# Optimization experiments

Hardware: AMD Instinct MI355X
Metric: run time of the kernel (lower is better)

Reference implementation:

```python
import jax, jax.numpy as jnp
import numpy as np

B, L, D, DI, DS, DC, DTR = 128, 31, 1024, 2048, 16, 5, 64

def setup_inputs() -> dict:
    key = jax.random.key(0)
    ks = jax.random.split(key, 12)
    rn = lambda k, shp, s=0.02: jax.random.normal(k, shp, dtype=jnp.float32) * s
    return {
        "x": jax.random.normal(ks[0], (B, L, D), dtype=jnp.float32),
        "norm1_w": jnp.ones((D,), jnp.float32), "norm1_b": jnp.zeros((D,), jnp.float32),
        "in_proj_W": rn(ks[1], (2 * DI, D)),
        "conv_w": rn(ks[2], (DI, DC), 0.2), "conv_b": jnp.zeros((DI,), jnp.float32),
        "x_proj_W": rn(ks[3], (DTR + 2 * DS, DI)),
        "dt_proj_W": rn(ks[4], (DI, DTR), 0.1),
        "dt_proj_b": jnp.full((DI,), -4.6, dtype=jnp.float32),  # softplus^-1(~0.01)
        "A_log": jnp.tile(jnp.log(jnp.arange(1, DS + 1, dtype=jnp.float32))[None, :], (DI, 1)),
        "D_ssm": jnp.ones((DI,), jnp.float32),
        "out_proj_W": rn(ks[5], (D, DI)),
        "norm2_w": jnp.ones((D,), jnp.float32), "norm2_b": jnp.zeros((D,), jnp.float32),
        "ffn_W1": rn(ks[6], (2 * D, D)), "ffn_b1": jnp.zeros((2 * D,), jnp.float32),
        "ffn_W2": rn(ks[7], (D, 2 * D)), "ffn_b2": jnp.zeros((D,), jnp.float32),
        "cls_W1": rn(ks[8], (D, L * D)), "cls_b1": jnp.zeros((D,), jnp.float32),
        "cls_W2": rn(ks[9], (1, D)), "cls_b2": jnp.zeros((1,), jnp.float32),
    }

def _ln(x, w, b):
    m = x.mean(-1, keepdims=True)
    v = x.var(-1, keepdims=True)
    return (x - m) * jax.lax.rsqrt(v + 1e-5) * w + b

def _mamba(x, in_proj_W, conv_w, conv_b, x_proj_W, dt_proj_W, dt_proj_b, A_log, D_ssm, out_proj_W):
    # in_proj -> (u, z)
    xz = jnp.einsum('bld,ed->ble', x, in_proj_W)            # (B,L,2*DI)
    u, z = jnp.split(xz, 2, axis=-1)
    # causal depthwise conv1d (kernel DC) + SiLU
    xp = jnp.pad(u, ((0, 0), (DC - 1, 0), (0, 0)))
    uc = conv_b + sum(xp[:, k:k + L, :] * conv_w[:, k] for k in range(DC))
    uc = jax.nn.silu(uc)
    # input-dependent dt, B, C
    x_dbl = jnp.einsum('bld,ed->ble', uc, x_proj_W)         # (B,L,DTR+2*DS)
    dt, Bm, Cm = jnp.split(x_dbl, [DTR, DTR + DS], axis=-1)
    dt = jax.nn.softplus(jnp.einsum('blr,dr->bld', dt, dt_proj_W) + dt_proj_b)
    A = -jnp.exp(A_log)                                      # (DI,DS)
    def step(h, ins):
        dt_t, B_t, C_t, u_t = ins                            # (B,DI),(B,DS),(B,DS),(B,DI)
        dA = jnp.exp(dt_t[:, :, None] * A)                   # (B,DI,DS)
        h = h * dA + dt_t[:, :, None] * B_t[:, None, :] * u_t[:, :, None]
        y = jnp.einsum('bds,bs->bd', h, C_t)
        return h, y
    h0 = jnp.zeros((u.shape[0], DI, DS), u.dtype)
    _, ys = jax.lax.scan(step, h0, (dt.transpose(1, 0, 2), Bm.transpose(1, 0, 2),
                                    Cm.transpose(1, 0, 2), uc.transpose(1, 0, 2)))
    y = ys.transpose(1, 0, 2) + uc * D_ssm                   # skip term D*u
    y = y * jax.nn.silu(z)                                   # gate
    return jnp.einsum('bld,ed->ble', y, out_proj_W)

def reference(x, norm1_w, norm1_b, in_proj_W, conv_w, conv_b, x_proj_W, dt_proj_W,
              dt_proj_b, A_log, D_ssm, out_proj_W, norm2_w, norm2_b, ffn_W1, ffn_b1,
              ffn_W2, ffn_b2, cls_W1, cls_b1, cls_W2, cls_b2):
    # single encoder block (n_layers=1), dropout = identity (eval)
    res = x
    h = _ln(x, norm1_w, norm1_b)
    h = _mamba(h, in_proj_W, conv_w, conv_b, x_proj_W, dt_proj_W, dt_proj_b,
               A_log, D_ssm, out_proj_W)
    x = res + h
    res = x
    h = _ln(x, norm2_w, norm2_b)
    h = jax.nn.silu(jnp.einsum('bld,ed->ble', h, ffn_W1) + ffn_b1)
    h = jnp.einsum('ble,de->bld', h, ffn_W2) + ffn_b2
    x = res + h
    # classifier: Flatten -> Linear -> SiLU -> Linear
    flat = x.reshape(x.shape[0], -1)                          # (B, L*D)
    c = jax.nn.silu(flat @ cls_W1.T + cls_b1)
    out = c @ cls_W2.T + cls_b2                               # (B,1)
    return (out, x)
```

## Files before the change

kernel.cpp:

```cpp
#include <hip/hip_runtime.h>
#include <cstddef>
#include <cstdint>

#define B_   128
#define L_   31
#define D_   1024
#define DI_  2048
#define DS_  16
#define DC_  5
#define DTR_ 64
#define ROWS (B_ * L_)
#define KCLS (L_ * D_)

typedef unsigned short u16;
typedef __attribute__((ext_vector_type(8))) short s16x8;
typedef __attribute__((ext_vector_type(4))) float f32x4;

__device__ __forceinline__ float silu_f(float x) { return x / (1.0f + __expf(-x)); }

__device__ __forceinline__ u16 f2b(float f) {
    union { float f; uint32_t u; } c; c.f = f;
    uint32_t u = c.u + 0x7FFF + ((c.u >> 16) & 1);
    return (u16)(u >> 16);
}
__device__ __forceinline__ float b2f(u16 b) {
    union { uint32_t u; float f; } c; c.u = ((uint32_t)b) << 16;
    return c.f;
}
__device__ __forceinline__ uint32_t pack2(float lo, float hi) {
    return (uint32_t)f2b(lo) | ((uint32_t)f2b(hi) << 16);
}

#define GLD16(g, s) __builtin_amdgcn_global_load_lds( \
    (const __attribute__((address_space(1))) void*)(g), \
    (__attribute__((address_space(3))) void*)(s), 16, 0, 0)

__global__ __launch_bounds__(256) void f2b_kernel(const float* __restrict__ in,
                                                  u16* __restrict__ out, int n8)
{
    int i = blockIdx.x * 256 + threadIdx.x;
    if (i >= n8) return;
    const float4* p = (const float4*)in + (size_t)i * 2;
    float4 a = p[0], b = p[1];
    uint4 r;
    r.x = pack2(a.x, a.y); r.y = pack2(a.z, a.w);
    r.z = pack2(b.x, b.y); r.w = pack2(b.z, b.w);
    ((uint4*)out)[i] = r;
}

__global__ __launch_bounds__(256) void ln_kernel(const float* __restrict__ x,
                                                 const float* __restrict__ w,
                                                 const float* __restrict__ b,
                                                 u16* __restrict__ y)
{
    const int row = blockIdx.x;
    const float* xr = x + (size_t)row * D_;
    float v[4];
    float sum = 0.f, sq = 0.f;
#pragma unroll
    for (int i = 0; i < 4; i++) {
        v[i] = xr[threadIdx.x + i * 256];
        sum += v[i];
        sq  += v[i] * v[i];
    }
#pragma unroll
    for (int o = 32; o > 0; o >>= 1) {
        sum += __shfl_down(sum, o, 64);
        sq  += __shfl_down(sq, o, 64);
    }
    __shared__ float red[8];
    const int wid = threadIdx.x >> 6;
    if ((threadIdx.x & 63) == 0) { red[wid] = sum; red[4 + wid] = sq; }
    __syncthreads();
    sum = red[0] + red[1] + red[2] + red[3];
    sq  = red[4] + red[5] + red[6] + red[7];
    const float mean = sum * (1.0f / D_);
    const float var  = sq * (1.0f / D_) - mean * mean;
    const float rstd = rsqrtf(var + 1e-5f);
    u16* yr = y + (size_t)row * D_;
#pragma unroll
    for (int i = 0; i < 4; i++) {
        const int c = threadIdx.x + i * 256;
        yr[c] = f2b((v[i] - mean) * rstd * w[c] + b[c]);
    }
}

template <int ACT, bool BIAS, bool RES, bool OUTB>
__global__ __launch_bounds__(256) void gemm_mfma(
    const u16* __restrict__ A, const u16* __restrict__ W,
    const float* __restrict__ bias, const float* __restrict__ res,
    void* __restrict__ Cout, int M, int K, int Nout)
{
    __shared__ __align__(16) u16 As[128 * 32];
    __shared__ __align__(16) u16 Bs[128 * 32];
    const int tid = threadIdx.x;
    const int l = tid & 63, w = tid >> 6;
    const int bm = blockIdx.y * 128, bn = blockIdx.x * 128;

    const int sr = l >> 2;
    const int sk = (l & 3) * 8;
    const u16* gA = A + (size_t)(bm + w * 16 + sr) * K + sk;
    const u16* gB = W + (size_t)(bn + w * 16 + sr) * K + sk;
    u16* lA = As + (w * 16 + sr) * 32 + sk;
    u16* lB = Bs + (w * 16 + sr) * 32 + sk;

    const int lane15 = l & 15, lhi = l >> 4;
    const int wr = w >> 1, wc = w & 1;
    const u16* fA = As + (wr * 64 + lane15) * 32 + lhi * 8;
    const u16* fB = Bs + (wc * 64 + lane15) * 32 + lhi * 8;

    f32x4 acc[4][4] = {};

    for (int k0 = 0; k0 < K; k0 += 32) {
        GLD16(gA, lA); GLD16(gA + (size_t)64 * K, lA + 64 * 32);
        GLD16(gB, lB); GLD16(gB + (size_t)64 * K, lB + 64 * 32);
        gA += 32; gB += 32;
        __syncthreads();
        s16x8 af[4], bfr[4];
#pragma unroll
        for (int mi = 0; mi < 4; mi++) af[mi]  = *(const s16x8*)(fA + mi * 16 * 32);
#pragma unroll
        for (int ni = 0; ni < 4; ni++) bfr[ni] = *(const s16x8*)(fB + ni * 16 * 32);
#pragma unroll
        for (int mi = 0; mi < 4; mi++)
#pragma unroll
            for (int ni = 0; ni < 4; ni++)
                acc[mi][ni] = __builtin_amdgcn_mfma_f32_16x16x32_bf16(
                    af[mi], bfr[ni], acc[mi][ni], 0, 0, 0);
        __syncthreads();
    }

#pragma unroll
    for (int ni = 0; ni < 4; ni++) {
        const int col = bn + wc * 64 + ni * 16 + lane15;
        if (col >= Nout) continue;
        const float bv = BIAS ? bias[col] : 0.0f;
#pragma unroll
        for (int mi = 0; mi < 4; mi++) {
#pragma unroll
            for (int r = 0; r < 4; r++) {
                const int row = bm + wr * 64 + mi * 16 + lhi * 4 + r;
                float v = acc[mi][ni][r] + bv;
                if (ACT == 1) v = silu_f(v);
                if (RES) v += res[(size_t)row * Nout + col];
                if (OUTB) ((u16*)Cout)[(size_t)row * Nout + col] = f2b(v);
                else      ((float*)Cout)[(size_t)row * Nout + col] = v;
            }
        }
    }
}

#define KCH 512
__global__ __launch_bounds__(256) void gemm_cls_mfma(
    const float* __restrict__ A, const float* __restrict__ W,
    float* __restrict__ C)
{
    __shared__ __align__(16) u16 As[128 * 32];
    __shared__ __align__(16) u16 Bs[128 * 32];
    const int tid = threadIdx.x;
    const int l = tid & 63, w = tid >> 6;
    const int bn = blockIdx.x * 128;
    const int k0 = blockIdx.y * KCH;

    const int sr = l >> 2;
    const int sk = (l & 3) * 8;
    const int row = w * 16 + sr;
    const float* gA0 = A + (size_t)row * KCLS + k0 + sk;
    const float* gA1 = gA0 + (size_t)64 * KCLS;
    const float* gB0 = W + (size_t)(bn + row) * KCLS + k0 + sk;
    const float* gB1 = gB0 + (size_t)64 * KCLS;
    u16* lA0 = As + row * 32 + sk;  u16* lA1 = lA0 + 64 * 32;
    u16* lB0 = Bs + row * 32 + sk;  u16* lB1 = lB0 + 64 * 32;

    const int lane15 = l & 15, lhi = l >> 4;
    const int wr = w >> 1, wc = w & 1;
    const u16* fA = As + (wr * 64 + lane15) * 32 + lhi * 8;
    const u16* fB = Bs + (wc * 64 + lane15) * 32 + lhi * 8;

    f32x4 acc[4][4] = {};

    for (int ks = 0; ks < KCH / 32; ks++) {
        float4 a00 = *(const float4*)(gA0);     float4 a01 = *(const float4*)(gA0 + 4);
        float4 a10 = *(const float4*)(gA1);     float4 a11 = *(const float4*)(gA1 + 4);
        float4 b00 = *(const float4*)(gB0);     float4 b01 = *(const float4*)(gB0 + 4);
        float4 b10 = *(const float4*)(gB1);     float4 b11 = *(const float4*)(gB1 + 4);
        gA0 += 32; gA1 += 32; gB0 += 32; gB1 += 32;
        __syncthreads();
        uint4 r;
        r.x = pack2(a00.x, a00.y); r.y = pack2(a00.z, a00.w);
        r.z = pack2(a01.x, a01.y); r.w = pack2(a01.z, a01.w);
        *(uint4*)lA0 = r;
        r.x = pack2(a10.x, a10.y); r.y = pack2(a10.z, a10.w);
        r.z = pack2(a11.x, a11.y); r.w = pack2(a11.z, a11.w);
        *(uint4*)lA1 = r;
        r.x = pack2(b00.x, b00.y); r.y = pack2(b00.z, b00.w);
        r.z = pack2(b01.x, b01.y); r.w = pack2(b01.z, b01.w);
        *(uint4*)lB0 = r;
        r.x = pack2(b10.x, b10.y); r.y = pack2(b10.z, b10.w);
        r.z = pack2(b11.x, b11.y); r.w = pack2(b11.z, b11.w);
        *(uint4*)lB1 = r;
        __syncthreads();
        s16x8 af[4], bfr[4];
#pragma unroll
        for (int mi = 0; mi < 4; mi++) af[mi]  = *(const s16x8*)(fA + mi * 16 * 32);
#pragma unroll
        for (int ni = 0; ni < 4; ni++) bfr[ni] = *(const s16x8*)(fB + ni * 16 * 32);
#pragma unroll
        for (int mi = 0; mi < 4; mi++)
#pragma unroll
            for (int ni = 0; ni < 4; ni++)
                acc[mi][ni] = __builtin_amdgcn_mfma_f32_16x16x32_bf16(
                    af[mi], bfr[ni], acc[mi][ni], 0, 0, 0);
    }

#pragma unroll
    for (int ni = 0; ni < 4; ni++) {
        const int col = bn + wc * 64 + ni * 16 + lane15;
#pragma unroll
        for (int mi = 0; mi < 4; mi++) {
#pragma unroll
            for (int r = 0; r < 4; r++) {
                const int m = wr * 64 + mi * 16 + lhi * 4 + r;
                atomicAdd(&C[(size_t)m * 1024 + col], acc[mi][ni][r]);
            }
        }
    }
}

template <int ACT, bool BIAS, bool OUTB>
__global__ __launch_bounds__(256) void gemm_f32(const float* __restrict__ A, int lda,
                                                const float* __restrict__ W,
                                                const float* __restrict__ bias,
                                                void* __restrict__ C,
                                                int M, int N, int K)
{
    const int bm = blockIdx.y * 64;
    const int bn = blockIdx.x * 64;
    const int tid = threadIdx.x;
    const int tx = tid & 15;
    const int ty = tid >> 4;
    const int lr = tid >> 2;
    const int lc = (tid & 3) << 2;
    __shared__ float As[16][64];
    __shared__ float Ws[16][64];
    float acc[4][4] = {};
    const int am = bm + lr;
    const int wn = bn + lr;

    for (int k0 = 0; k0 < K; k0 += 16) {
        float4 av = make_float4(0.f, 0.f, 0.f, 0.f);
        float4 wv = make_float4(0.f, 0.f, 0.f, 0.f);
        if (am < M) av = *(const float4*)(A + (size_t)am * lda + k0 + lc);
        if (wn < N) wv = *(const float4*)(W + (size_t)wn * K + k0 + lc);
        __syncthreads();
        As[lc + 0][lr] = av.x; As[lc + 1][lr] = av.y; As[lc + 2][lr] = av.z; As[lc + 3][lr] = av.w;
        Ws[lc + 0][lr] = wv.x; Ws[lc + 1][lr] = wv.y; Ws[lc + 2][lr] = wv.z; Ws[lc + 3][lr] = wv.w;
        __syncthreads();
#pragma unroll
        for (int k = 0; k < 16; k++) {
            float a[4], wv2[4];
#pragma unroll
            for (int i = 0; i < 4; i++) a[i] = As[k][ty * 4 + i];
#pragma unroll
            for (int j = 0; j < 4; j++) wv2[j] = Ws[k][tx * 4 + j];
#pragma unroll
            for (int i = 0; i < 4; i++)
#pragma unroll
                for (int j = 0; j < 4; j++)
                    acc[i][j] = fmaf(a[i], wv2[j], acc[i][j]);
        }
    }

#pragma unroll
    for (int i = 0; i < 4; i++) {
        const int m = bm + ty * 4 + i;
        if (m >= M) continue;
#pragma unroll
        for (int j = 0; j < 4; j++) {
            const int n = bn + tx * 4 + j;
            if (n >= N) continue;
            float v = acc[i][j];
            if (BIAS) v += bias[n];
            if (ACT == 2) v = (v > 20.0f) ? v : log1pf(__expf(v));
            if (OUTB) ((u16*)C)[(size_t)m * N + n] = f2b(v);
            else      ((float*)C)[(size_t)m * N + n] = v;
        }
    }
}

__global__ __launch_bounds__(256) void conv_silu_kernel(const u16* __restrict__ xz,
                                                        const float* __restrict__ cw,
                                                        const float* __restrict__ cb,
                                                        u16* __restrict__ uc)
{
    const int idx = blockIdx.x * 256 + threadIdx.x;
    const int d  = idx & (DI_ - 1);
    const int bl = idx >> 11;
    const int l  = bl % L_;
    const int b  = bl / L_;
    const u16* u = xz + (size_t)b * L_ * (2 * DI_) + d;
    float acc = cb[d];
#pragma unroll
    for (int k = 0; k < DC_; k++) {
        const int ll = l + k - (DC_ - 1);
        if (ll >= 0) acc = fmaf(b2f(u[(size_t)ll * (2 * DI_)]), cw[d * DC_ + k], acc);
    }
    uc[(size_t)bl * DI_ + d] = f2b(silu_f(acc));
}

__global__ __launch_bounds__(256) void scan_kernel(const u16* __restrict__ dt,
                                                   const u16* __restrict__ uc,
                                                   const u16* __restrict__ xz,
                                                   const float* __restrict__ xdbl,
                                                   const float* __restrict__ A_log,
                                                   const float* __restrict__ D_ssm,
                                                   u16* __restrict__ y)
{
    const int idx = blockIdx.x * 256 + threadIdx.x;
    const int d = idx & (DI_ - 1);
    const int b = idx >> 11;
    float A[DS_];
#pragma unroll
    for (int s = 0; s < DS_; s++) A[s] = -__expf(A_log[d * DS_ + s]);
    const float Dv = D_ssm[d];
    float h[DS_] = {};
    for (int l = 0; l < L_; l++) {
        const size_t bl = (size_t)b * L_ + l;
        const float dtv = b2f(dt[bl * DI_ + d]);
        const float uv  = b2f(uc[bl * DI_ + d]);
        const float zv  = b2f(xz[bl * (2 * DI_) + DI_ + d]);
        const float* Bp = xdbl + bl * (DTR_ + 2 * DS_) + DTR_;
        const float* Cp = Bp + DS_;
        float yv = 0.f;
#pragma unroll
        for (int s = 0; s < DS_; s++) {
            h[s] = fmaf(h[s], __expf(dtv * A[s]), dtv * Bp[s] * uv);
            yv = fmaf(h[s], Cp[s], yv);
        }
        yv = fmaf(uv, Dv, yv);
        yv *= silu_f(zv);
        y[bl * DI_ + d] = f2b(yv);
    }
}

__global__ __launch_bounds__(256) void cls2_kernel(const float* __restrict__ c,
                                                   const float* __restrict__ b1,
                                                   const float* __restrict__ W2,
                                                   const float* __restrict__ b2,
                                                   float* __restrict__ out)
{
    const int b = blockIdx.x;
    float s = 0.f;
    for (int n = threadIdx.x; n < D_; n += 256) {
        float v = c[b * D_ + n] + b1[n];
        v = silu_f(v);
        s = fmaf(v, W2[n], s);
    }
#pragma unroll
    for (int o = 32; o > 0; o >>= 1) s += __shfl_down(s, o, 64);
    __shared__ float red[4];
    const int wid = threadIdx.x >> 6;
    if ((threadIdx.x & 63) == 0) red[wid] = s;
    __syncthreads();
    if (threadIdx.x == 0) out[b] = red[0] + red[1] + red[2] + red[3] + b2[0];
}

extern "C" void kernel_launch(void* const* d_in, const int* in_sizes, int n_in,
                              void* d_out, int out_size, void* d_ws, size_t ws_size,
                              hipStream_t stream)
{
    const float* x         = (const float*)d_in[0];
    const float* n1w       = (const float*)d_in[1];
    const float* n1b       = (const float*)d_in[2];
    const float* in_projW  = (const float*)d_in[3];
    const float* conv_w    = (const float*)d_in[4];
    const float* conv_b    = (const float*)d_in[5];
    const float* x_projW   = (const float*)d_in[6];
    const float* dt_projW  = (const float*)d_in[7];
    const float* dt_projb  = (const float*)d_in[8];
    const float* A_log     = (const float*)d_in[9];
    const float* D_ssm     = (const float*)d_in[10];
    const float* out_projW = (const float*)d_in[11];
    const float* n2w       = (const float*)d_in[12];
    const float* n2b       = (const float*)d_in[13];
    const float* ffn_W1    = (const float*)d_in[14];
    const float* ffn_b1    = (const float*)d_in[15];
    const float* ffn_W2    = (const float*)d_in[16];
    const float* ffn_b2    = (const float*)d_in[17];
    const float* cls_W1    = (const float*)d_in[18];
    const float* cls_b1    = (const float*)d_in[19];
    const float* cls_W2    = (const float*)d_in[20];
    const float* cls_b2    = (const float*)d_in[21];

    float* ws   = (float*)d_ws;
    u16*   xz_b = (u16*)ws;
    u16*   uc_b = xz_b + (size_t)ROWS * 4096;
    u16*   dt_b = uc_b + (size_t)ROWS * 2048;
    u16*   y_b  = dt_b + (size_t)ROWS * 2048;
    u16*   h_b  = y_b + (size_t)ROWS * 2048;
    float* x2   = (float*)(h_b + (size_t)ROWS * 1024);
    float* xdbl = x2 + (size_t)ROWS * 1024;
    u16*   wbuf = (u16*)(xdbl + (size_t)ROWS * 96);
    float* clsh = (float*)(wbuf + (size_t)4096 * 1024);

    float* outv = (float*)d_out;
    float* x3   = outv + B_;

    ln_kernel<<<dim3(ROWS), dim3(256), 0, stream>>>(x, n1w, n1b, h_b);
    f2b_kernel<<<dim3(4096 * 1024 / 8 / 256), dim3(256), 0, stream>>>(in_projW, wbuf, 4096 * 1024 / 8);
    gemm_mfma<0, false, false, true><<<dim3(4096 / 128, ROWS / 128), dim3(256), 0, stream>>>(
        h_b, wbuf, nullptr, nullptr, xz_b, ROWS, D_, 2 * DI_);
    conv_silu_kernel<<<dim3(ROWS * DI_ / 256), dim3(256), 0, stream>>>(xz_b, conv_w, conv_b, uc_b);
    hipMemsetAsync(wbuf, 0, (size_t)128 * 2048 * sizeof(u16), stream);
    f2b_kernel<<<dim3(96 * 2048 / 8 / 256), dim3(256), 0, stream>>>(x_projW, wbuf, 96 * 2048 / 8);
    gemm_mfma<0, false, false, false><<<dim3(1, ROWS / 128), dim3(256), 0, stream>>>(
        uc_b, wbuf, nullptr, nullptr, xdbl, ROWS, DI_, DTR_ + 2 * DS_);
    gemm_f32<2, true, true><<<dim3(2048 / 64, ROWS / 64), dim3(256), 0, stream>>>(
        xdbl, DTR_ + 2 * DS_, dt_projW, dt_projb, dt_b, ROWS, DI_, DTR_);
    scan_kernel<<<dim3(B_ * DI_ / 256), dim3(256), 0, stream>>>(
        dt_b, uc_b, xz_b, xdbl, A_log, D_ssm, y_b);
    f2b_kernel<<<dim3(1024 * 2048 / 8 / 256), dim3(256), 0, stream>>>(out_projW, wbuf, 1024 * 2048 / 8);
    gemm_mfma<0, false, true, false><<<dim3(1024 / 128, ROWS / 128), dim3(256), 0, stream>>>(
        y_b, wbuf, nullptr, x, x2, ROWS, DI_, D_);
    ln_kernel<<<dim3(ROWS), dim3(256), 0, stream>>>(x2, n2w, n2b, h_b);
    f2b_kernel<<<dim3(2048 * 1024 / 8 / 256), dim3(256), 0, stream>>>(ffn_W1, wbuf, 2048 * 1024 / 8);
    gemm_mfma<1, true, false, true><<<dim3(2048 / 128, ROWS / 128), dim3(256), 0, stream>>>(
        h_b, wbuf, ffn_b1, nullptr, uc_b, ROWS, D_, 2 * D_);
    f2b_kernel<<<dim3(1024 * 2048 / 8 / 256), dim3(256), 0, stream>>>(ffn_W2, wbuf, 1024 * 2048 / 8);
    gemm_mfma<0, true, true, false><<<dim3(1024 / 128, ROWS / 128), dim3(256), 0, stream>>>(
        uc_b, wbuf, ffn_b2, x2, x3, ROWS, 2 * D_, D_);
    hipMemsetAsync(clsh, 0, (size_t)B_ * D_ * sizeof(float), stream);
    gemm_cls_mfma<<<dim3(1024 / 128, KCLS / KCH), dim3(256), 0, stream>>>(x3, cls_W1, clsh);
    cls2_kernel<<<dim3(B_), dim3(256), 0, stream>>>(clsh, cls_b1, cls_W2, cls_b2, outv);
}
```

Baseline: 473.5 us.

## Batch weight conversions, split-K x_proj GEMM, and run dt_proj on MFMA

Converts all projection weights to bf16 in a single launch instead of one conversion kernel per GEMM. The x_proj GEMM is split along K into four chunks accumulated with atomics, to raise parallelism beyond 31 blocks. dt_proj moves from a scalar fp32 tiled GEMM to the bf16 MFMA GEMM with a softplus epilogue, using a small extraction kernel that packs dt to bf16. This adds atomic accumulation plus an extra memset, and lowers dt_proj input precision to bf16.

```diff
diff --git a/kernel.cpp b/kernel.cpp
--- a/kernel.cpp
+++ b/kernel.cpp
@@ -12,6 +12,14 @@
 #define ROWS (B_ * L_)
 #define KCLS (L_ * D_)
 
+#define W_IN  0
+#define W_OUT 4194304
+#define W_F1  6291456
+#define W_F2  8388608
+#define W_XP  10485760
+#define W_DT  10747904
+#define WTOT  10878976
+
 typedef unsigned short u16;
 typedef __attribute__((ext_vector_type(8))) short s16x8;
 typedef __attribute__((ext_vector_type(4))) float f32x4;
@@ -30,22 +38,43 @@
 __device__ __forceinline__ uint32_t pack2(float lo, float hi) {
     return (uint32_t)f2b(lo) | ((uint32_t)f2b(hi) << 16);
 }
-
-#define GLD16(g, s) __builtin_amdgcn_global_load_lds( \
-    (const __attribute__((address_space(1))) void*)(g), \
-    (__attribute__((address_space(3))) void*)(s), 16, 0, 0)
-
-__global__ __launch_bounds__(256) void f2b_kernel(const float* __restrict__ in,
-                                                  u16* __restrict__ out, int n8)
-{
-    int i = blockIdx.x * 256 + threadIdx.x;
-    if (i >= n8) return;
-    const float4* p = (const float4*)in + (size_t)i * 2;
+__device__ __forceinline__ void cvt8(const float* __restrict__ s, u16* __restrict__ d) {
+    const float4* p = (const float4*)s;
     float4 a = p[0], b = p[1];
     uint4 r;
     r.x = pack2(a.x, a.y); r.y = pack2(a.z, a.w);
     r.z = pack2(b.x, b.y); r.w = pack2(b.z, b.w);
-    ((uint4*)out)[i] = r;
+    *(uint4*)d = r;
+}
+
+#define GLD16(g, s) __builtin_amdgcn_global_load_lds( \
+    (const __attribute__((address_space(1))) void*)(g), \
+    (__attribute__((address_space(3))) void*)(s), 16, 0, 0)
+
+__global__ __launch_bounds__(256) void f2b_all_kernel(
+    const float* __restrict__ inW, const float* __restrict__ outW,
+    const float* __restrict__ f1W, const float* __restrict__ f2W,
+    const float* __restrict__ xpW, const float* __restrict__ dtW,
+    u16* __restrict__ wbuf)
+{
+    int g = blockIdx.x * 256 + threadIdx.x;
+    if (g < 524288) { cvt8(inW + (size_t)g * 8, wbuf + W_IN + (size_t)g * 8); return; }
+    g -= 524288;
+    if (g < 262144) { cvt8(outW + (size_t)g * 8, wbuf + W_OUT + (size_t)g * 8); return; }
+    g -= 262144;
+    if (g < 262144) { cvt8(f1W + (size_t)g * 8, wbuf + W_F1 + (size_t)g * 8); return; }
+    g -= 262144;
+    if (g < 262144) { cvt8(f2W + (size_t)g * 8, wbuf + W_F2 + (size_t)g * 8); return; }
+    g -= 262144;
+    if (g < 32768) {
+        const int row = g >> 8, col8 = (g & 255) * 8;
+        u16* d = wbuf + W_XP + (size_t)row * 2048 + col8;
+        if (row < 96) cvt8(xpW + (size_t)row * 2048 + col8, d);
+        else *(uint4*)d = make_uint4(0, 0, 0, 0);
+        return;
+    }
+    g -= 32768;
+    if (g < 16384) cvt8(dtW + (size_t)g * 8, wbuf + W_DT + (size_t)g * 8);
 }
 
 __global__ __launch_bounds__(256) void ln_kernel(const float* __restrict__ x,
@@ -85,22 +114,23 @@
     }
 }
 
-template <int ACT, bool BIAS, bool RES, bool OUTB>
+template <int ACT, bool BIAS, bool RES, int OUT>
 __global__ __launch_bounds__(256) void gemm_mfma(
     const u16* __restrict__ A, const u16* __restrict__ W,
     const float* __restrict__ bias, const float* __restrict__ res,
-    void* __restrict__ Cout, int M, int K, int Nout)
+    void* __restrict__ Cout, int M, int K, int Nout, int kLen)
 {
     __shared__ __align__(16) u16 As[128 * 32];
     __shared__ __align__(16) u16 Bs[128 * 32];
     const int tid = threadIdx.x;
     const int l = tid & 63, w = tid >> 6;
     const int bm = blockIdx.y * 128, bn = blockIdx.x * 128;
+    const int kOff = blockIdx.z * kLen;
 
     const int sr = l >> 2;
     const int sk = (l & 3) * 8;
-    const u16* gA = A + (size_t)(bm + w * 16 + sr) * K + sk;
-    const u16* gB = W + (size_t)(bn + w * 16 + sr) * K + sk;
+    const u16* gA = A + (size_t)(bm + w * 16 + sr) * K + kOff + sk;
+    const u16* gB = W + (size_t)(bn + w * 16 + sr) * K + kOff + sk;
     u16* lA = As + (w * 16 + sr) * 32 + sk;
     u16* lB = Bs + (w * 16 + sr) * 32 + sk;
 
@@ -111,7 +141,7 @@
 
     f32x4 acc[4][4] = {};
 
-    for (int k0 = 0; k0 < K; k0 += 32) {
+    for (int kk = 0; kk < kLen; kk += 32) {
         GLD16(gA, lA); GLD16(gA + (size_t)64 * K, lA + 64 * 32);
         GLD16(gB, lB); GLD16(gB + (size_t)64 * K, lB + 64 * 32);
         gA += 32; gB += 32;
@@ -142,9 +172,11 @@
                 const int row = bm + wr * 64 + mi * 16 + lhi * 4 + r;
                 float v = acc[mi][ni][r] + bv;
                 if (ACT == 1) v = silu_f(v);
+                if (ACT == 2) v = (v > 20.0f) ? v : log1pf(__expf(v));
                 if (RES) v += res[(size_t)row * Nout + col];
-                if (OUTB) ((u16*)Cout)[(size_t)row * Nout + col] = f2b(v);
-                else      ((float*)Cout)[(size_t)row * Nout + col] = v;
+                if (OUT == 0) ((float*)Cout)[(size_t)row * Nout + col] = v;
+                if (OUT == 1) ((u16*)Cout)[(size_t)row * Nout + col] = f2b(v);
+                if (OUT == 2) atomicAdd(&((float*)Cout)[(size_t)row * Nout + col], v);
             }
         }
     }
@@ -227,67 +259,6 @@
     }
 }
 
-template <int ACT, bool BIAS, bool OUTB>
-__global__ __launch_bounds__(256) void gemm_f32(const float* __restrict__ A, int lda,
-                                                const float* __restrict__ W,
-                                                const float* __restrict__ bias,
-                                                void* __restrict__ C,
-                                                int M, int N, int K)
-{
-    const int bm = blockIdx.y * 64;
-    const int bn = blockIdx.x * 64;
-    const int tid = threadIdx.x;
-    const int tx = tid & 15;
-    const int ty = tid >> 4;
-    const int lr = tid >> 2;
-    const int lc = (tid & 3) << 2;
-    __shared__ float As[16][64];
-    __shared__ float Ws[16][64];
-    float acc[4][4] = {};
-    const int am = bm + lr;
-    const int wn = bn + lr;
-
-    for (int k0 = 0; k0 < K; k0 += 16) {
-        float4 av = make_float4(0.f, 0.f, 0.f, 0.f);
-        float4 wv = make_float4(0.f, 0.f, 0.f, 0.f);
-        if (am < M) av = *(const float4*)(A + (size_t)am * lda + k0 + lc);
-        if (wn < N) wv = *(const float4*)(W + (size_t)wn * K + k0 + lc);
-        __syncthreads();
-        As[lc + 0][lr] = av.x; As[lc + 1][lr] = av.y; As[lc + 2][lr] = av.z; As[lc + 3][lr] = av.w;
-        Ws[lc + 0][lr] = wv.x; Ws[lc + 1][lr] = wv.y; Ws[lc + 2][lr] = wv.z; Ws[lc + 3][lr] = wv.w;
-        __syncthreads();
-#pragma unroll
-        for (int k = 0; k < 16; k++) {
-            float a[4], wv2[4];
-#pragma unroll
-            for (int i = 0; i < 4; i++) a[i] = As[k][ty * 4 + i];
-#pragma unroll
-            for (int j = 0; j < 4; j++) wv2[j] = Ws[k][tx * 4 + j];
-#pragma unroll
-            for (int i = 0; i < 4; i++)
-#pragma unroll
-                for (int j = 0; j < 4; j++)
-                    acc[i][j] = fmaf(a[i], wv2[j], acc[i][j]);
-        }
-    }
-
-#pragma unroll
-    for (int i = 0; i < 4; i++) {
-        const int m = bm + ty * 4 + i;
-        if (m >= M) continue;
-#pragma unroll
-        for (int j = 0; j < 4; j++) {
-            const int n = bn + tx * 4 + j;
-            if (n >= N) continue;
-            float v = acc[i][j];
-            if (BIAS) v += bias[n];
-            if (ACT == 2) v = (v > 20.0f) ? v : log1pf(__expf(v));
-            if (OUTB) ((u16*)C)[(size_t)m * N + n] = f2b(v);
-            else      ((float*)C)[(size_t)m * N + n] = v;
-        }
-    }
-}
-
 __global__ __launch_bounds__(256) void conv_silu_kernel(const u16* __restrict__ xz,
                                                         const float* __restrict__ cw,
                                                         const float* __restrict__ cb,
@@ -306,6 +277,17 @@
         if (ll >= 0) acc = fmaf(b2f(u[(size_t)ll * (2 * DI_)]), cw[d * DC_ + k], acc);
     }
     uc[(size_t)bl * DI_ + d] = f2b(silu_f(acc));
+}
+
+__global__ __launch_bounds__(256) void dtext_kernel(const float* __restrict__ xdbl,
+                                                    u16* __restrict__ dtb)
+{
+    const int idx = blockIdx.x * 256 + threadIdx.x;
+    const int row = idx >> 4, c4 = (idx & 15) * 4;
+    float4 v = *(const float4*)(xdbl + (size_t)row * 96 + c4);
+    uint2 r;
+    r.x = pack2(v.x, v.y); r.y = pack2(v.z, v.w);
+    *(uint2*)(dtb + (size_t)row * 64 + c4) = r;
 }
 
 __global__ __launch_bounds__(256) void scan_kernel(const u16* __restrict__ dt,
@@ -400,35 +382,34 @@
     u16*   h_b  = y_b + (size_t)ROWS * 2048;
     float* x2   = (float*)(h_b + (size_t)ROWS * 1024);
     float* xdbl = x2 + (size_t)ROWS * 1024;
-    u16*   wbuf = (u16*)(xdbl + (size_t)ROWS * 96);
-    float* clsh = (float*)(wbuf + (size_t)4096 * 1024);
+    u16*   dtb  = (u16*)(xdbl + (size_t)ROWS * 96);
+    u16*   wbuf = dtb + (size_t)ROWS * 64;
+    float* clsh = (float*)(wbuf + (size_t)WTOT);
 
     float* outv = (float*)d_out;
     float* x3   = outv + B_;
 
+    f2b_all_kernel<<<dim3(5312), dim3(256), 0, stream>>>(
+        in_projW, out_projW, ffn_W1, ffn_W2, x_projW, dt_projW, wbuf);
     ln_kernel<<<dim3(ROWS), dim3(256), 0, stream>>>(x, n1w, n1b, h_b);
-    f2b_kernel<<<dim3(4096 * 1024 / 8 / 256), dim3(256), 0, stream>>>(in_projW, wbuf, 4096 * 1024 / 8);
-    gemm_mfma<0, false, false, true><<<dim3(4096 / 128, ROWS / 128), dim3(256), 0, stream>>>(
-        h_b, wbuf, nullptr, nullptr, xz_b, ROWS, D_, 2 * DI_);
+    gemm_mfma<0, false, false, 1><<<dim3(32, 31, 1), dim3(256), 0, stream>>>(
+        h_b, wbuf + W_IN, nullptr, nullptr, xz_b, ROWS, D_, 2 * DI_, D_);
     conv_silu_kernel<<<dim3(ROWS * DI_ / 256), dim3(256), 0, stream>>>(xz_b, conv_w, conv_b, uc_b);
-    hipMemsetAsync(wbuf, 0, (size_t)128 * 2048 * sizeof(u16), stream);
-    f2b_kernel<<<dim3(96 * 2048 / 8 / 256), dim3(256), 0, stream>>>(x_projW, wbuf, 96 * 2048 / 8);
-    gemm_mfma<0, false, false, false><<<dim3(1, ROWS / 128), dim3(256), 0, stream>>>(
-        uc_b, wbuf, nullptr, nullptr, xdbl, ROWS, DI_, DTR_ + 2 * DS_);
-    gemm_f32<2, true, true><<<dim3(2048 / 64, ROWS / 64), dim3(256), 0, stream>>>(
-        xdbl, DTR_ + 2 * DS_, dt_projW, dt_projb, dt_b, ROWS, DI_, DTR_);
+    hipMemsetAsync(xdbl, 0, (size_t)ROWS * 96 * sizeof(float), stream);
+    gemm_mfma<0, false, false, 2><<<dim3(1, 31, 4), dim3(256), 0, stream>>>(
+        uc_b, wbuf + W_XP, nullptr, nullptr, xdbl, ROWS, DI_, DTR_ + 2 * DS_, 512);
+    dtext_kernel<<<dim3(ROWS * 16 / 256), dim3(256), 0, stream>>>(xdbl, dtb);
+    gemm_mfma<2, true, false, 1><<<dim3(16, 31, 1), dim3(256), 0, stream>>>(
+        dtb, wbuf + W_DT, dt_projb, nullptr, dt_b, ROWS, DTR_, DI_, DTR_);
     scan_kernel<<<dim3(B_ * DI_ / 256), dim3(256), 0, stream>>>(
         dt_b, uc_b, xz_b, xdbl, A_log, D_ssm, y_b);
-    f2b_kernel<<<dim3(1024 * 2048 / 8 / 256), dim3(256), 0, stream>>>(out_projW, wbuf, 1024 * 2048 / 8);
-    gemm_mfma<0, false, true, false><<<dim3(1024 / 128, ROWS / 128), dim3(256), 0, stream>>>(
-        y_b, wbuf, nullptr, x, x2, ROWS, DI_, D_);
+    gemm_mfma<0, false, true, 0><<<dim3(8, 31, 1), dim3(256), 0, stream>>>(
+        y_b, wbuf + W_OUT, nullptr, x, x2, ROWS, DI_, D_, DI_);
     ln_kernel<<<dim3(ROWS), dim3(256), 0, stream>>>(x2, n2w, n2b, h_b);
-    f2b_kernel<<<dim3(2048 * 1024 / 8 / 256), dim3(256), 0, stream>>>(ffn_W1, wbuf, 2048 * 1024 / 8);
-    gemm_mfma<1, true, false, true><<<dim3(2048 / 128, ROWS / 128), dim3(256), 0, stream>>>(
-        h_b, wbuf, ffn_b1, nullptr, uc_b, ROWS, D_, 2 * D_);
-    f2b_kernel<<<dim3(1024 * 2048 / 8 / 256), dim3(256), 0, stream>>>(ffn_W2, wbuf, 1024 * 2048 / 8);
-    gemm_mfma<0, true, true, false><<<dim3(1024 / 128, ROWS / 128), dim3(256), 0, stream>>>(
-        uc_b, wbuf, ffn_b2, x2, x3, ROWS, 2 * D_, D_);
+    gemm_mfma<1, true, false, 1><<<dim3(16, 31, 1), dim3(256), 0, stream>>>(
+        h_b, wbuf + W_F1, ffn_b1, nullptr, uc_b, ROWS, D_, 2 * D_, D_);
+    gemm_mfma<0, true, true, 0><<<dim3(8, 31, 1), dim3(256), 0, stream>>>(
+        uc_b, wbuf + W_F2, ffn_b2, x2, x3, ROWS, 2 * D_, D_, 2 * D_);
     hipMemsetAsync(clsh, 0, (size_t)B_ * D_ * sizeof(float), stream);
     gemm_cls_mfma<<<dim3(1024 / 128, KCLS / KCH), dim3(256), 0, stream>>>(x3, cls_W1, clsh);
     cls2_kernel<<<dim3(B_), dim3(256), 0, stream>>>(clsh, cls_b1, cls_W2, cls_b2, outv);
```

Result: faster. 437.5 us (-7.6%).
